# Optimization experiments

Measured on AMD Instinct MI355X. Metric: run time of the kernel, lower is better.

The kernel has to match this reference:

```python
import jax, jax.numpy as jnp
import numpy as np

N_CELL, N_NET, N_GCELL = 50000, 10000, 20000
E = 100000
D = 32   # hidden_node = hidden_net = hidden_hanna = out_node = out_net
DP = 16  # hidden_pin = hidden_edge feats


def setup_inputs() -> dict:
    key = jax.random.key(0)
    ks = jax.random.split(key, 21)
    f = jax.random.normal
    ri = lambda k, n: jax.random.randint(k, (E,), 0, n, dtype=jnp.int32)
    return {
        'node_feat': f(ks[0], (N_CELL, D), jnp.float32),
        'net_feat': f(ks[1], (N_NET, D), jnp.float32),
        'pin_feat': f(ks[2], (E, DP), jnp.float32),
        'hanna_feat': f(ks[3], (N_GCELL, D), jnp.float32),
        'edge_feat': f(ks[4], (E, DP), jnp.float32),
        'pins_src': ri(ks[5], N_CELL), 'pins_dst': ri(ks[6], N_NET),
        'pinned_src': ri(ks[7], N_NET), 'pinned_dst': ri(ks[8], N_CELL),
        'connect_src': ri(ks[9], N_GCELL), 'connect_dst': ri(ks[10], N_GCELL),
        'pt_src': ri(ks[11], N_CELL), 'pt_dst': ri(ks[12], N_GCELL),
        'pf_src': ri(ks[13], N_GCELL), 'pf_dst': ri(ks[14], N_CELL),
        'W_net': f(ks[15], (D, D)) * 0.1, 'b_net': jnp.zeros((D,), jnp.float32),
        'W_topo': f(ks[16], (DP, D * D)) * 0.1, 'b_topo': jnp.zeros((D * D,), jnp.float32),
        'W_pins': f(ks[17], (D, D)) * 0.1, 'b_pins': jnp.zeros((D,), jnp.float32),
        'W_connect': f(ks[18], (D, D)) * 0.1, 'b_connect': jnp.zeros((D,), jnp.float32),
        'W_pt': f(ks[19], (D, D)) * 0.1, 'b_pt': jnp.zeros((D,), jnp.float32),
        'b_pinned': jnp.zeros((D,), jnp.float32), 'b_pf': jnp.zeros((D,), jnp.float32),
    }


def _deg(idx, n):
    # clamped degree, as DGL clamps to min 1
    return jnp.maximum(jax.ops.segment_sum(jnp.ones_like(idx, jnp.float32), idx, n), 1.0)


def graph_conv(h_src, W, b, src, dst, n_src, n_dst):
    # DGL GraphConv with norm='both': D_out^{-1/2} gather -> sum -> D_in^{-1/2}, then W, b
    feat = (h_src * _deg(src, n_src)[:, None] ** -0.5) @ W
    agg = jax.ops.segment_sum(feat[src], dst, n_dst)
    return agg * _deg(dst, n_dst)[:, None] ** -0.5 + b


def nn_conv(h_src, efeat, W_topo, b_topo, bias, src, dst, n_dst):
    # DGL NNConv (aggregator='mean'): per-edge weight from edge_func, mean over in-edges
    d_in = h_src.shape[1]
    w = (efeat @ W_topo + b_topo).reshape(-1, d_in, bias.shape[0])  # (E, d_in, d_out)
    m = jnp.einsum('ei,eio->eo', h_src[src], w)
    return jax.ops.segment_sum(m, dst, n_dst) / _deg(dst, n_dst)[:, None] + bias


def reference(node_feat, net_feat, pin_feat, hanna_feat, edge_feat,
              pins_src, pins_dst, pinned_src, pinned_dst, connect_src, connect_dst,
              pt_src, pt_dst, pf_src, pf_dst,
              W_net, b_net, W_topo, b_topo, W_pins, b_pins,
              W_connect, b_connect, W_pt, b_pt, b_pinned, b_pf):
    # 'pins': cell -> net (GraphConv)
    h_net = graph_conv(node_feat, W_pins, b_pins, pins_src, pins_dst, N_CELL, N_NET)
    # 'pinned': net -> cell (NNConv) + 'point-from': gcell -> cell (NNConv); agg='sum'
    h_cell = (nn_conv(net_feat, pin_feat, W_topo, b_topo, b_pinned, pinned_src, pinned_dst, N_CELL)
              + nn_conv(hanna_feat, edge_feat, W_topo, b_topo, b_pf, pf_src, pf_dst, N_CELL))
    # 'connect': gcell -> gcell + 'point-to': cell -> gcell (GraphConvs); agg='sum'
    h_gcell = (graph_conv(hanna_feat, W_connect, b_connect, connect_src, connect_dst, N_GCELL, N_GCELL)
               + graph_conv(node_feat, W_pt, b_pt, pt_src, pt_dst, N_CELL, N_GCELL))
    return (h_cell, h_net + net_feat @ W_net + b_net, h_gcell)
```

## Files before the change

### kernel.cpp

```cpp
#include <hip/hip_runtime.h>

typedef unsigned short u16;
typedef unsigned int u32;

#define NC 50000
#define NN 10000
#define NG 20000
#define NE 100000
#define NSCAN 150016
#define NBLK 74


__device__ __forceinline__ float bflo(u32 a) { return __uint_as_float(a << 16); }
__device__ __forceinline__ float bfhi(u32 a) { return __uint_as_float(a & 0xFFFF0000u); }
__device__ __forceinline__ u16 fbf(float f) {
  u32 u = __float_as_uint(f);
  return (u16)((u + 0x7FFFu + ((u >> 16) & 1u)) >> 16);
}

__device__ __forceinline__ float nn_msg(int e, int s, const float* __restrict__ ef,
                                        const u16* __restrict__ T,
                                        const float* __restrict__ C, int o) {
  const float4* efp = reinterpret_cast<const float4*>(ef + (size_t)e * 16);
  float4 ea = efp[0], eb = efp[1], ec = efp[2], ed = efp[3];
  const uint4* tp = reinterpret_cast<const uint4*>(T + (size_t)s * 512 + o * 16);
  uint4 ta = tp[0], tb = tp[1];
  float m = C[(size_t)s * 32 + o];
  m += ea.x * bflo(ta.x) + ea.y * bfhi(ta.x) + ea.z * bflo(ta.y) + ea.w * bfhi(ta.y);
  m += eb.x * bflo(ta.z) + eb.y * bfhi(ta.z) + eb.z * bflo(ta.w) + eb.w * bfhi(ta.w);
  m += ec.x * bflo(tb.x) + ec.y * bfhi(tb.x) + ec.z * bflo(tb.y) + ec.w * bfhi(tb.y);
  m += ed.x * bflo(tb.z) + ed.y * bfhi(tb.z) + ed.z * bflo(tb.w) + ed.w * bfhi(tb.w);
  return m;
}

__global__ __launch_bounds__(512) void k_front(
    const float* __restrict__ feat_net, const float* __restrict__ feat_han,
    const float* __restrict__ W_topo, const float* __restrict__ b_topo,
    u16* __restrict__ T_net, u16* __restrict__ T_han,
    float* __restrict__ C_net, float* __restrict__ C_han,
    const int* __restrict__ pins_src, const int* __restrict__ pins_dst,
    const int* __restrict__ pinned_dst, const int* __restrict__ pf_dst,
    const int* __restrict__ connect_src, const int* __restrict__ connect_dst,
    const int* __restrict__ pt_src, const int* __restrict__ pt_dst,
    int* __restrict__ hist, int* __restrict__ srccnt) {
  int b = blockIdx.x;
  int tid = threadIdx.x;
  if (b < 938) {
    __shared__ float hs[4][32];
    bool han = b >= 313;
    const float* feat = han ? feat_han : feat_net;
    u16* T = han ? T_han : T_net;
    int n = han ? NG : NN;
    int blk = han ? (b - 313) : b;
    int j = tid;
    int p = j & 15, o = j >> 4;
    float w[32];
#pragma unroll
    for (int i = 0; i < 32; i++) w[i] = W_topo[p * 1024 + i * 32 + o];
    int s0 = blk * 32;
    int s1 = min(s0 + 32, n);
    for (int s = s0; s < s1; s += 4) {
      __syncthreads();
      if (tid < 128) {
        int r = tid >> 5, i = tid & 31;
        int sn = s + r;
        hs[r][i] = (sn < s1) ? feat[(size_t)sn * 32 + i] : 0.f;
      }
      __syncthreads();
#pragma unroll
      for (int r = 0; r < 4; r++) {
        int sn = s + r;
        if (sn >= s1) break;
        float acc = 0.f;
#pragma unroll
        for (int i = 0; i < 32; i++) acc += hs[r][i] * w[i];
        T[(size_t)sn * 512 + j] = fbf(acc);
      }
    }
    return;
  }
  if (b < 2813) {
    int t = (b - 938) * 512 + tid;
    int s2 = t >> 5, o = t & 31;
    bool han = s2 >= NN;
    const float* feat = han ? feat_han : feat_net;
    float* C = han ? C_han : C_net;
    int s = han ? s2 - NN : s2;
    float acc = 0.f;
#pragma unroll 8
    for (int i = 0; i < 32; i++)
      acc += feat[(size_t)s * 32 + i] * b_topo[i * 32 + o];
    C[(size_t)s * 32 + o] = acc;
    return;
  }
  int e = (b - 2813) * 512 + tid;
  if (e >= NE) return;
  atomicAdd(&hist[pins_dst[e]], 1);
  atomicAdd(&hist[10000 + connect_dst[e]], 1);
  atomicAdd(&hist[30000 + pt_dst[e]], 1);
  atomicAdd(&hist[50000 + pinned_dst[e]], 1);
  atomicAdd(&hist[100000 + pf_dst[e]], 1);
  atomicAdd(&srccnt[pins_src[e]], 1);
  atomicAdd(&srccnt[50000 + connect_src[e]], 1);
  atomicAdd(&srccnt[70000 + pt_src[e]], 1);
}

__global__ __launch_bounds__(256) void k_scan(
    const int* __restrict__ cnt, int* __restrict__ bases,
    int* __restrict__ cursor) {
  __shared__ int sm[256];
  __shared__ int carryS;
  int b = blockIdx.x, tid = threadIdx.x;
  int lim = b * 2048;
  int part = 0;
  for (int i = tid * 4; i < lim; i += 1024) {
    int4 v = *reinterpret_cast<const int4*>(cnt + i);
    part += v.x + v.y + v.z + v.w;
  }
  sm[tid] = part;
  __syncthreads();
  for (int off = 128; off > 0; off >>= 1) {
    if (tid < off) sm[tid] += sm[tid + off];
    __syncthreads();
  }
  if (tid == 0) carryS = sm[0];
  __syncthreads();
  int base = b * 2048 + tid * 8;
  int v[8];
  int tot = 0;
#pragma unroll
  for (int j = 0; j < 8; j++) {
    int i = base + j;
    v[j] = (i < NSCAN) ? cnt[i] : 0;
    tot += v[j];
  }
  sm[tid] = tot;
  __syncthreads();
  for (int off = 1; off < 256; off <<= 1) {
    int add = (tid >= off) ? sm[tid - off] : 0;
    __syncthreads();
    sm[tid] += add;
    __syncthreads();
  }
  int excl = sm[tid] - tot + carryS;
#pragma unroll
  for (int j = 0; j < 8; j++) {
    int i = base + j;
    if (i < NSCAN) { bases[i] = excl; cursor[i] = excl; }
    excl += v[j];
  }
}

__global__ __launch_bounds__(512) void k_fill(
    const int* __restrict__ pins_src, const int* __restrict__ pins_dst,
    const int* __restrict__ connect_src, const int* __restrict__ connect_dst,
    const int* __restrict__ pt_src, const int* __restrict__ pt_dst,
    const int* __restrict__ pinned_src, const int* __restrict__ pinned_dst,
    const int* __restrict__ pf_src, const int* __restrict__ pf_dst,
    const int* __restrict__ srccnt, int* __restrict__ cursor,
    int2* __restrict__ csr_gc, int2* __restrict__ csr_nn) {
  int t = blockIdx.x * 512 + threadIdx.x;
  if (t >= 5 * NE) return;
  int r = (t >= NE) + (t >= 2 * NE) + (t >= 3 * NE) + (t >= 4 * NE);
  int e = t - r * NE;
  const int* srcs = r == 0 ? pins_src : r == 1 ? connect_src
                   : r == 2 ? pt_src : r == 3 ? pinned_src : pf_src;
  const int* dsts = r == 0 ? pins_dst : r == 1 ? connect_dst
                   : r == 2 ? pt_dst : r == 3 ? pinned_dst : pf_dst;
  int off = r == 0 ? 0 : r == 1 ? 10000 : r == 2 ? 30000 : r == 3 ? 50000 : 100000;
  int s = srcs[e];
  int g = off + dsts[e];
  int pos = atomicAdd(&cursor[g], 1);
  if (r < 3) {
    int soff = r == 0 ? 0 : r == 1 ? 50000 : 70000;
    float w = rsqrtf(fmaxf((float)srccnt[soff + s], 1.f));
    csr_gc[pos] = make_int2(s, __float_as_int(w));
  } else {
    csr_nn[pos - 300000] = make_int2(e, s);
  }
}

__global__ __launch_bounds__(512) void k_big(
    const int* __restrict__ hist, const int* __restrict__ bases,
    const int2* __restrict__ csr_gc, const int2* __restrict__ csr_nn,
    const float* __restrict__ node_feat, const float* __restrict__ hanna_feat,
    const float* __restrict__ net_feat,
    const float* __restrict__ pin_feat, const float* __restrict__ edge_feat,
    const u16* __restrict__ T_net, const u16* __restrict__ T_han,
    const float* __restrict__ C_net, const float* __restrict__ C_han,
    const float* __restrict__ b_pinned, const float* __restrict__ b_pf,
    const float* __restrict__ W_pins, const float* __restrict__ b_pins,
    const float* __restrict__ W_net, const float* __restrict__ b_net,
    const float* __restrict__ W_connect, const float* __restrict__ b_connect,
    const float* __restrict__ W_pt, const float* __restrict__ b_pt,
    float* __restrict__ out) {
  __shared__ float Wa[1024], Wb[1024];
  __shared__ float srow[16][32];
  int b = blockIdx.x, tid = threadIdx.x;
  if (b < 3125) {
    int t = b * 512 + tid;
    int d = t >> 5, o = t & 31;
    float a0 = 0.f, a1 = 0.f;
    {
      int g = 50000 + d;
      int base = bases[g] - 300000, deg = hist[g];
      int k = 0;
      for (; k + 1 < deg; k += 2) {
        int2 ea = csr_nn[base + k], eb = csr_nn[base + k + 1];
        a0 += nn_msg(ea.x, ea.y, pin_feat, T_net, C_net, o) +
              nn_msg(eb.x, eb.y, pin_feat, T_net, C_net, o);
      }
      if (k < deg) {
        int2 ea = csr_nn[base + k];
        a0 += nn_msg(ea.x, ea.y, pin_feat, T_net, C_net, o);
      }
      a0 /= fmaxf((float)deg, 1.f);
    }
    {
      int g = 100000 + d;
      int base = bases[g] - 300000, deg = hist[g];
      int k = 0;
      for (; k + 1 < deg; k += 2) {
        int2 ea = csr_nn[base + k], eb = csr_nn[base + k + 1];
        a1 += nn_msg(ea.x, ea.y, edge_feat, T_han, C_han, o) +
              nn_msg(eb.x, eb.y, edge_feat, T_han, C_han, o);
      }
      if (k < deg) {
        int2 ea = csr_nn[base + k];
        a1 += nn_msg(ea.x, ea.y, edge_feat, T_han, C_han, o);
      }
      a1 /= fmaxf((float)deg, 1.f);
    }
    out[(size_t)d * 32 + o] = a0 + a1 + b_pinned[o] + b_pf[o];
    return;
  }
  if (b < 3750) {
    int bb = b - 3125;
    for (int k = tid; k < 1024; k += 512) {
      Wa[k] = W_pins[k];
      Wb[k] = W_net[k];
    }
    int rl = tid >> 5, o = tid & 31;
    int r = bb * 16 + rl;
    int base = bases[r], deg = hist[r];
    float acc = 0.f;
    int k = 0;
    for (; k + 1 < deg; k += 2) {
      int2 pa = csr_gc[base + k], pb = csr_gc[base + k + 1];
      acc += node_feat[(size_t)pa.x * 32 + o] * __int_as_float(pa.y) +
             node_feat[(size_t)pb.x * 32 + o] * __int_as_float(pb.y);
    }
    if (k < deg) {
      int2 pa = csr_gc[base + k];
      acc += node_feat[(size_t)pa.x * 32 + o] * __int_as_float(pa.y);
    }
    srow[rl][o] = acc;
    __syncthreads();
    float a1 = 0.f, a2 = 0.f;
#pragma unroll 8
    for (int i = 0; i < 32; i++) {
      a1 += srow[rl][i] * Wa[i * 32 + o];
      a2 += net_feat[(size_t)r * 32 + i] * Wb[i * 32 + o];
    }
    out[1600000 + (size_t)r * 32 + o] =
        a1 * rsqrtf(fmaxf((float)deg, 1.f)) + b_pins[o] + a2 + b_net[o];
    return;
  }
  int bb = b - 3750;
  for (int k = tid; k < 1024; k += 512) {
    Wa[k] = W_connect[k];
    Wb[k] = W_pt[k];
  }
  int rl = tid >> 6;
  int half = (tid >> 5) & 1;
  int o = tid & 31;
  int r = bb * 8 + rl;
  int g = (half ? 30000 : 10000) + r;
  const float* feat = half ? node_feat : hanna_feat;
  int base = bases[g], deg = hist[g];
  float acc = 0.f;
  int k = 0;
  for (; k + 1 < deg; k += 2) {
    int2 pa = csr_gc[base + k], pb = csr_gc[base + k + 1];
    acc += feat[(size_t)pa.x * 32 + o] * __int_as_float(pa.y) +
           feat[(size_t)pb.x * 32 + o] * __int_as_float(pb.y);
  }
  if (k < deg) {
    int2 pa = csr_gc[base + k];
    acc += feat[(size_t)pa.x * 32 + o] * __int_as_float(pa.y);
  }
  srow[rl * 2 + half][o] = acc;
  __syncthreads();
  if (half == 0) {
    float a1 = 0.f, a2 = 0.f;
#pragma unroll 8
    for (int i = 0; i < 32; i++) {
      a1 += srow[rl * 2 + 0][i] * Wa[i * 32 + o];
      a2 += srow[rl * 2 + 1][i] * Wb[i * 32 + o];
    }
    out[1920000 + (size_t)r * 32 + o] =
        a1 * rsqrtf(fmaxf((float)hist[10000 + r], 1.f)) + b_connect[o] +
        a2 * rsqrtf(fmaxf((float)hist[30000 + r], 1.f)) + b_pt[o];
  }
}

extern "C" void kernel_launch(void* const* d_in, const int* in_sizes, int n_in,
                              void* d_out, int out_size, void* d_ws, size_t ws_size,
                              hipStream_t stream) {
  const float* node_feat  = (const float*)d_in[0];
  const float* net_feat   = (const float*)d_in[1];
  const float* pin_feat   = (const float*)d_in[2];
  const float* hanna_feat = (const float*)d_in[3];
  const float* edge_feat  = (const float*)d_in[4];
  const int* pins_src    = (const int*)d_in[5];
  const int* pins_dst    = (const int*)d_in[6];
  const int* pinned_src  = (const int*)d_in[7];
  const int* pinned_dst  = (const int*)d_in[8];
  const int* connect_src = (const int*)d_in[9];
  const int* connect_dst = (const int*)d_in[10];
  const int* pt_src      = (const int*)d_in[11];
  const int* pt_dst      = (const int*)d_in[12];
  const int* pf_src      = (const int*)d_in[13];
  const int* pf_dst      = (const int*)d_in[14];
  const float* W_net     = (const float*)d_in[15];
  const float* b_net     = (const float*)d_in[16];
  const float* W_topo    = (const float*)d_in[17];
  const float* b_topo    = (const float*)d_in[18];
  const float* W_pins    = (const float*)d_in[19];
  const float* b_pins    = (const float*)d_in[20];
  const float* W_connect = (const float*)d_in[21];
  const float* b_connect = (const float*)d_in[22];
  const float* W_pt      = (const float*)d_in[23];
  const float* b_pt      = (const float*)d_in[24];
  const float* b_pinned  = (const float*)d_in[25];
  const float* b_pf      = (const float*)d_in[26];
  float* out = (float*)d_out;

  int* wi = (int*)d_ws;
  int* hist    = wi + 0;
  int* srccnt  = wi + 150016;
  int* bases   = wi + 270032;
  int* cursor  = wi + 420048;
  int2* csr_gc = (int2*)(wi + 570064);
  int2* csr_nn = (int2*)(wi + 1170064);
  float* wf = (float*)d_ws;
  float* C_net  = wf + 1570064;
  float* C_han  = wf + 1890064;
  u16* T_net = (u16*)((char*)d_ws + 10120256);
  u16* T_han = (u16*)((char*)d_ws + 10120256 + 10240000);

  hipMemsetAsync(d_ws, 0, 270032 * sizeof(int), stream);

  k_front<<<3009, 512, 0, stream>>>(
      net_feat, hanna_feat, W_topo, b_topo, T_net, T_han, C_net, C_han,
      pins_src, pins_dst, pinned_dst, pf_dst, connect_src, connect_dst,
      pt_src, pt_dst, hist, srccnt);

  k_scan<<<NBLK, 256, 0, stream>>>(hist, bases, cursor);

  k_fill<<<(5 * NE + 511) / 512, 512, 0, stream>>>(
      pins_src, pins_dst, connect_src, connect_dst, pt_src, pt_dst,
      pinned_src, pinned_dst, pf_src, pf_dst, srccnt, cursor,
      csr_gc, csr_nn);

  k_big<<<6250, 512, 0, stream>>>(
      hist, bases, csr_gc, csr_nn, node_feat, hanna_feat, net_feat,
      pin_feat, edge_feat, T_net, T_han, C_net, C_han, b_pinned, b_pf,
      W_pins, b_pins, W_net, b_net, W_connect, b_connect, W_pt, b_pt, out);
}
```

Baseline: 323.2 us.

## Fuse four kernels into one persistent kernel with grid-wide barriers

Replaces the four kernel launches (front, scan, fill, big) with one persistent kernel of 512 blocks that loops over the former block indices and separates the phases with an atomic-counter grid barrier. The aim is to remove per-launch overhead and the idle tails between dependent kernels. The scan now uses 512 threads with 4 elements each, and the two NNConv aggregation loops are interleaved in one loop. The barrier assumes all 512 blocks are resident at once, which launch_bounds(512,4) is meant to allow. Fixing the grid at 512 blocks of 512 threads may lower occupancy in the gather-heavy final phase.

```diff
diff --git a/kernel.cpp b/kernel.cpp
--- a/kernel.cpp
+++ b/kernel.cpp
@@ -9,6 +9,7 @@
 #define NE 100000
 #define NSCAN 150016
 #define NBLK 74
+#define NGRID 512
 
 
 __device__ __forceinline__ float bflo(u32 a) { return __uint_as_float(a << 16); }
@@ -33,274 +34,261 @@
   return m;
 }
 
-__global__ __launch_bounds__(512) void k_front(
-    const float* __restrict__ feat_net, const float* __restrict__ feat_han,
-    const float* __restrict__ W_topo, const float* __restrict__ b_topo,
-    u16* __restrict__ T_net, u16* __restrict__ T_han,
-    float* __restrict__ C_net, float* __restrict__ C_han,
+__device__ __forceinline__ void gbar(int* cnt) {
+  __syncthreads();
+  if (threadIdx.x == 0) {
+    __threadfence();
+    atomicAdd(cnt, 1);
+    while (atomicAdd(cnt, 0) < NGRID) __builtin_amdgcn_s_sleep(8);
+  }
+  __syncthreads();
+  __threadfence();
+}
+
+__global__ __launch_bounds__(512, 4) void k_mega(
+    const float* __restrict__ node_feat, const float* __restrict__ net_feat,
+    const float* __restrict__ pin_feat, const float* __restrict__ hanna_feat,
+    const float* __restrict__ edge_feat,
     const int* __restrict__ pins_src, const int* __restrict__ pins_dst,
-    const int* __restrict__ pinned_dst, const int* __restrict__ pf_dst,
+    const int* __restrict__ pinned_src, const int* __restrict__ pinned_dst,
     const int* __restrict__ connect_src, const int* __restrict__ connect_dst,
     const int* __restrict__ pt_src, const int* __restrict__ pt_dst,
-    int* __restrict__ hist, int* __restrict__ srccnt) {
-  int b = blockIdx.x;
-  int tid = threadIdx.x;
-  if (b < 938) {
-    __shared__ float hs[4][32];
-    bool han = b >= 313;
-    const float* feat = han ? feat_han : feat_net;
-    u16* T = han ? T_han : T_net;
-    int n = han ? NG : NN;
-    int blk = han ? (b - 313) : b;
-    int j = tid;
-    int p = j & 15, o = j >> 4;
-    float w[32];
-#pragma unroll
-    for (int i = 0; i < 32; i++) w[i] = W_topo[p * 1024 + i * 32 + o];
-    int s0 = blk * 32;
-    int s1 = min(s0 + 32, n);
-    for (int s = s0; s < s1; s += 4) {
-      __syncthreads();
-      if (tid < 128) {
-        int r = tid >> 5, i = tid & 31;
-        int sn = s + r;
-        hs[r][i] = (sn < s1) ? feat[(size_t)sn * 32 + i] : 0.f;
-      }
-      __syncthreads();
-#pragma unroll
-      for (int r = 0; r < 4; r++) {
-        int sn = s + r;
-        if (sn >= s1) break;
-        float acc = 0.f;
-#pragma unroll
-        for (int i = 0; i < 32; i++) acc += hs[r][i] * w[i];
-        T[(size_t)sn * 512 + j] = fbf(acc);
-      }
-    }
-    return;
-  }
-  if (b < 2813) {
-    int t = (b - 938) * 512 + tid;
-    int s2 = t >> 5, o = t & 31;
-    bool han = s2 >= NN;
-    const float* feat = han ? feat_han : feat_net;
-    float* C = han ? C_han : C_net;
-    int s = han ? s2 - NN : s2;
-    float acc = 0.f;
-#pragma unroll 8
-    for (int i = 0; i < 32; i++)
-      acc += feat[(size_t)s * 32 + i] * b_topo[i * 32 + o];
-    C[(size_t)s * 32 + o] = acc;
-    return;
-  }
-  int e = (b - 2813) * 512 + tid;
-  if (e >= NE) return;
-  atomicAdd(&hist[pins_dst[e]], 1);
-  atomicAdd(&hist[10000 + connect_dst[e]], 1);
-  atomicAdd(&hist[30000 + pt_dst[e]], 1);
-  atomicAdd(&hist[50000 + pinned_dst[e]], 1);
-  atomicAdd(&hist[100000 + pf_dst[e]], 1);
-  atomicAdd(&srccnt[pins_src[e]], 1);
-  atomicAdd(&srccnt[50000 + connect_src[e]], 1);
-  atomicAdd(&srccnt[70000 + pt_src[e]], 1);
-}
-
-__global__ __launch_bounds__(256) void k_scan(
-    const int* __restrict__ cnt, int* __restrict__ bases,
-    int* __restrict__ cursor) {
-  __shared__ int sm[256];
-  __shared__ int carryS;
-  int b = blockIdx.x, tid = threadIdx.x;
-  int lim = b * 2048;
-  int part = 0;
-  for (int i = tid * 4; i < lim; i += 1024) {
-    int4 v = *reinterpret_cast<const int4*>(cnt + i);
-    part += v.x + v.y + v.z + v.w;
-  }
-  sm[tid] = part;
-  __syncthreads();
-  for (int off = 128; off > 0; off >>= 1) {
-    if (tid < off) sm[tid] += sm[tid + off];
-    __syncthreads();
-  }
-  if (tid == 0) carryS = sm[0];
-  __syncthreads();
-  int base = b * 2048 + tid * 8;
-  int v[8];
-  int tot = 0;
-#pragma unroll
-  for (int j = 0; j < 8; j++) {
-    int i = base + j;
-    v[j] = (i < NSCAN) ? cnt[i] : 0;
-    tot += v[j];
-  }
-  sm[tid] = tot;
-  __syncthreads();
-  for (int off = 1; off < 256; off <<= 1) {
-    int add = (tid >= off) ? sm[tid - off] : 0;
-    __syncthreads();
-    sm[tid] += add;
-    __syncthreads();
-  }
-  int excl = sm[tid] - tot + carryS;
-#pragma unroll
-  for (int j = 0; j < 8; j++) {
-    int i = base + j;
-    if (i < NSCAN) { bases[i] = excl; cursor[i] = excl; }
-    excl += v[j];
-  }
-}
-
-__global__ __launch_bounds__(512) void k_fill(
-    const int* __restrict__ pins_src, const int* __restrict__ pins_dst,
-    const int* __restrict__ connect_src, const int* __restrict__ connect_dst,
-    const int* __restrict__ pt_src, const int* __restrict__ pt_dst,
-    const int* __restrict__ pinned_src, const int* __restrict__ pinned_dst,
     const int* __restrict__ pf_src, const int* __restrict__ pf_dst,
-    const int* __restrict__ srccnt, int* __restrict__ cursor,
-    int2* __restrict__ csr_gc, int2* __restrict__ csr_nn) {
-  int t = blockIdx.x * 512 + threadIdx.x;
-  if (t >= 5 * NE) return;
-  int r = (t >= NE) + (t >= 2 * NE) + (t >= 3 * NE) + (t >= 4 * NE);
-  int e = t - r * NE;
-  const int* srcs = r == 0 ? pins_src : r == 1 ? connect_src
-                   : r == 2 ? pt_src : r == 3 ? pinned_src : pf_src;
-  const int* dsts = r == 0 ? pins_dst : r == 1 ? connect_dst
-                   : r == 2 ? pt_dst : r == 3 ? pinned_dst : pf_dst;
-  int off = r == 0 ? 0 : r == 1 ? 10000 : r == 2 ? 30000 : r == 3 ? 50000 : 100000;
-  int s = srcs[e];
-  int g = off + dsts[e];
-  int pos = atomicAdd(&cursor[g], 1);
-  if (r < 3) {
-    int soff = r == 0 ? 0 : r == 1 ? 50000 : 70000;
-    float w = rsqrtf(fmaxf((float)srccnt[soff + s], 1.f));
-    csr_gc[pos] = make_int2(s, __float_as_int(w));
-  } else {
-    csr_nn[pos - 300000] = make_int2(e, s);
-  }
-}
-
-__global__ __launch_bounds__(512) void k_big(
-    const int* __restrict__ hist, const int* __restrict__ bases,
-    const int2* __restrict__ csr_gc, const int2* __restrict__ csr_nn,
-    const float* __restrict__ node_feat, const float* __restrict__ hanna_feat,
-    const float* __restrict__ net_feat,
-    const float* __restrict__ pin_feat, const float* __restrict__ edge_feat,
-    const u16* __restrict__ T_net, const u16* __restrict__ T_han,
-    const float* __restrict__ C_net, const float* __restrict__ C_han,
-    const float* __restrict__ b_pinned, const float* __restrict__ b_pf,
+    const float* __restrict__ W_net, const float* __restrict__ b_net,
+    const float* __restrict__ W_topo, const float* __restrict__ b_topo,
     const float* __restrict__ W_pins, const float* __restrict__ b_pins,
-    const float* __restrict__ W_net, const float* __restrict__ b_net,
     const float* __restrict__ W_connect, const float* __restrict__ b_connect,
     const float* __restrict__ W_pt, const float* __restrict__ b_pt,
+    const float* __restrict__ b_pinned, const float* __restrict__ b_pf,
+    int* __restrict__ hist, int* __restrict__ srccnt, int* __restrict__ bar,
+    int* __restrict__ bases, int* __restrict__ cursor,
+    int2* __restrict__ csr_gc, int2* __restrict__ csr_nn,
+    float* __restrict__ C_net, float* __restrict__ C_han,
+    u16* __restrict__ T_net, u16* __restrict__ T_han,
     float* __restrict__ out) {
+  __shared__ float hs[4][32];
+  __shared__ int smi[512];
   __shared__ float Wa[1024], Wb[1024];
   __shared__ float srow[16][32];
-  int b = blockIdx.x, tid = threadIdx.x;
-  if (b < 3125) {
-    int t = b * 512 + tid;
-    int d = t >> 5, o = t & 31;
-    float a0 = 0.f, a1 = 0.f;
-    {
-      int g = 50000 + d;
-      int base = bases[g] - 300000, deg = hist[g];
+  int tid = threadIdx.x;
+
+  for (int vb = blockIdx.x; vb < 3009; vb += NGRID) {
+    if (vb < 938) {
+      bool han = vb >= 313;
+      const float* feat = han ? hanna_feat : net_feat;
+      u16* T = han ? T_han : T_net;
+      int n = han ? NG : NN;
+      int blk = han ? (vb - 313) : vb;
+      int j = tid;
+      int p = j & 15, o = j >> 4;
+      float w[32];
+#pragma unroll
+      for (int i = 0; i < 32; i++) w[i] = W_topo[p * 1024 + i * 32 + o];
+      int s0 = blk * 32;
+      int s1 = min(s0 + 32, n);
+      for (int s = s0; s < s1; s += 4) {
+        __syncthreads();
+        if (tid < 128) {
+          int r = tid >> 5, i = tid & 31;
+          int sn = s + r;
+          hs[r][i] = (sn < s1) ? feat[(size_t)sn * 32 + i] : 0.f;
+        }
+        __syncthreads();
+#pragma unroll
+        for (int r = 0; r < 4; r++) {
+          int sn = s + r;
+          if (sn >= s1) break;
+          float acc = 0.f;
+#pragma unroll
+          for (int i = 0; i < 32; i++) acc += hs[r][i] * w[i];
+          T[(size_t)sn * 512 + j] = fbf(acc);
+        }
+      }
+    } else if (vb < 2813) {
+      int t = (vb - 938) * 512 + tid;
+      int s2 = t >> 5, o = t & 31;
+      bool han = s2 >= NN;
+      const float* feat = han ? hanna_feat : net_feat;
+      float* C = han ? C_han : C_net;
+      int s = han ? s2 - NN : s2;
+      float acc = 0.f;
+#pragma unroll 8
+      for (int i = 0; i < 32; i++)
+        acc += feat[(size_t)s * 32 + i] * b_topo[i * 32 + o];
+      C[(size_t)s * 32 + o] = acc;
+    } else {
+      int e = (vb - 2813) * 512 + tid;
+      if (e < NE) {
+        atomicAdd(&hist[pins_dst[e]], 1);
+        atomicAdd(&hist[10000 + connect_dst[e]], 1);
+        atomicAdd(&hist[30000 + pt_dst[e]], 1);
+        atomicAdd(&hist[50000 + pinned_dst[e]], 1);
+        atomicAdd(&hist[100000 + pf_dst[e]], 1);
+        atomicAdd(&srccnt[pins_src[e]], 1);
+        atomicAdd(&srccnt[50000 + connect_src[e]], 1);
+        atomicAdd(&srccnt[70000 + pt_src[e]], 1);
+      }
+    }
+  }
+  gbar(&bar[0]);
+
+  for (int vb = blockIdx.x; vb < NBLK; vb += NGRID) {
+    int lim = vb * 2048;
+    int part = 0;
+    for (int i = tid * 4; i < lim; i += 2048) {
+      int4 v = *reinterpret_cast<const int4*>(hist + i);
+      part += v.x + v.y + v.z + v.w;
+    }
+    smi[tid] = part;
+    __syncthreads();
+    for (int off = 256; off > 0; off >>= 1) {
+      if (tid < off) smi[tid] += smi[tid + off];
+      __syncthreads();
+    }
+    int carry = smi[0];
+    __syncthreads();
+    int base = vb * 2048 + tid * 4;
+    int v[4];
+    int tot = 0;
+#pragma unroll
+    for (int j = 0; j < 4; j++) {
+      int i = base + j;
+      v[j] = (i < NSCAN) ? hist[i] : 0;
+      tot += v[j];
+    }
+    smi[tid] = tot;
+    __syncthreads();
+    for (int off = 1; off < 512; off <<= 1) {
+      int add = (tid >= off) ? smi[tid - off] : 0;
+      __syncthreads();
+      smi[tid] += add;
+      __syncthreads();
+    }
+    int excl = smi[tid] - tot + carry;
+#pragma unroll
+    for (int j = 0; j < 4; j++) {
+      int i = base + j;
+      if (i < NSCAN) { bases[i] = excl; cursor[i] = excl; }
+      excl += v[j];
+    }
+  }
+  gbar(&bar[1]);
+
+  for (int vb = blockIdx.x; vb < 977; vb += NGRID) {
+    int t = vb * 512 + tid;
+    if (t < 5 * NE) {
+      int r = (t >= NE) + (t >= 2 * NE) + (t >= 3 * NE) + (t >= 4 * NE);
+      int e = t - r * NE;
+      const int* srcs = r == 0 ? pins_src : r == 1 ? connect_src
+                       : r == 2 ? pt_src : r == 3 ? pinned_src : pf_src;
+      const int* dsts = r == 0 ? pins_dst : r == 1 ? connect_dst
+                       : r == 2 ? pt_dst : r == 3 ? pinned_dst : pf_dst;
+      int off = r == 0 ? 0 : r == 1 ? 10000 : r == 2 ? 30000
+              : r == 3 ? 50000 : 100000;
+      int s = srcs[e];
+      int g = off + dsts[e];
+      int pos = atomicAdd(&cursor[g], 1);
+      if (r < 3) {
+        int soff = r == 0 ? 0 : r == 1 ? 50000 : 70000;
+        float w = rsqrtf(fmaxf((float)srccnt[soff + s], 1.f));
+        csr_gc[pos] = make_int2(s, __float_as_int(w));
+      } else {
+        csr_nn[pos - 300000] = make_int2(e, s);
+      }
+    }
+  }
+  gbar(&bar[2]);
+
+  for (int vb = blockIdx.x; vb < 6250; vb += NGRID) {
+    if (vb < 3125) {
+      int t = vb * 512 + tid;
+      int d = t >> 5, o = t & 31;
+      int g0 = 50000 + d, g1 = 100000 + d;
+      int b0 = bases[g0] - 300000, d0 = hist[g0];
+      int b1 = bases[g1] - 300000, d1 = hist[g1];
+      float a0 = 0.f, a1 = 0.f;
+      int kmax = max(d0, d1);
+      for (int k = 0; k < kmax; k++) {
+        int2 ea = make_int2(0, 0), eb = make_int2(0, 0);
+        bool h0 = k < d0, h1 = k < d1;
+        if (h0) ea = csr_nn[b0 + k];
+        if (h1) eb = csr_nn[b1 + k];
+        if (h0) a0 += nn_msg(ea.x, ea.y, pin_feat, T_net, C_net, o);
+        if (h1) a1 += nn_msg(eb.x, eb.y, edge_feat, T_han, C_han, o);
+      }
+      a0 /= fmaxf((float)d0, 1.f);
+      a1 /= fmaxf((float)d1, 1.f);
+      out[(size_t)d * 32 + o] = a0 + a1 + b_pinned[o] + b_pf[o];
+    } else if (vb < 3750) {
+      __syncthreads();
+      int bb = vb - 3125;
+      for (int k = tid; k < 1024; k += 512) {
+        Wa[k] = W_pins[k];
+        Wb[k] = W_net[k];
+      }
+      int rl = tid >> 5, o = tid & 31;
+      int r = bb * 16 + rl;
+      int base = bases[r], deg = hist[r];
+      float acc = 0.f;
       int k = 0;
       for (; k + 1 < deg; k += 2) {
-        int2 ea = csr_nn[base + k], eb = csr_nn[base + k + 1];
-        a0 += nn_msg(ea.x, ea.y, pin_feat, T_net, C_net, o) +
-              nn_msg(eb.x, eb.y, pin_feat, T_net, C_net, o);
+        int2 pa = csr_gc[base + k], pb = csr_gc[base + k + 1];
+        acc += node_feat[(size_t)pa.x * 32 + o] * __int_as_float(pa.y) +
+               node_feat[(size_t)pb.x * 32 + o] * __int_as_float(pb.y);
       }
       if (k < deg) {
-        int2 ea = csr_nn[base + k];
-        a0 += nn_msg(ea.x, ea.y, pin_feat, T_net, C_net, o);
-      }
-      a0 /= fmaxf((float)deg, 1.f);
-    }
-    {
-      int g = 100000 + d;
-      int base = bases[g] - 300000, deg = hist[g];
+        int2 pa = csr_gc[base + k];
+        acc += node_feat[(size_t)pa.x * 32 + o] * __int_as_float(pa.y);
+      }
+      srow[rl][o] = acc;
+      __syncthreads();
+      float a1 = 0.f, a2 = 0.f;
+#pragma unroll 8
+      for (int i = 0; i < 32; i++) {
+        a1 += srow[rl][i] * Wa[i * 32 + o];
+        a2 += net_feat[(size_t)r * 32 + i] * Wb[i * 32 + o];
+      }
+      out[1600000 + (size_t)r * 32 + o] =
+          a1 * rsqrtf(fmaxf((float)deg, 1.f)) + b_pins[o] + a2 + b_net[o];
+    } else {
+      __syncthreads();
+      int bb = vb - 3750;
+      for (int k = tid; k < 1024; k += 512) {
+        Wa[k] = W_connect[k];
+        Wb[k] = W_pt[k];
+      }
+      int rl = tid >> 6;
+      int half = (tid >> 5) & 1;
+      int o = tid & 31;
+      int r = bb * 8 + rl;
+      int g = (half ? 30000 : 10000) + r;
+      const float* feat = half ? node_feat : hanna_feat;
+      int base = bases[g], deg = hist[g];
+      float acc = 0.f;
       int k = 0;
       for (; k + 1 < deg; k += 2) {
-        int2 ea = csr_nn[base + k], eb = csr_nn[base + k + 1];
-        a1 += nn_msg(ea.x, ea.y, edge_feat, T_han, C_han, o) +
-              nn_msg(eb.x, eb.y, edge_feat, T_han, C_han, o);
+        int2 pa = csr_gc[base + k], pb = csr_gc[base + k + 1];
+        acc += feat[(size_t)pa.x * 32 + o] * __int_as_float(pa.y) +
+               feat[(size_t)pb.x * 32 + o] * __int_as_float(pb.y);
       }
       if (k < deg) {
-        int2 ea = csr_nn[base + k];
-        a1 += nn_msg(ea.x, ea.y, edge_feat, T_han, C_han, o);
-      }
-      a1 /= fmaxf((float)deg, 1.f);
-    }
-    out[(size_t)d * 32 + o] = a0 + a1 + b_pinned[o] + b_pf[o];
-    return;
-  }
-  if (b < 3750) {
-    int bb = b - 3125;
-    for (int k = tid; k < 1024; k += 512) {
-      Wa[k] = W_pins[k];
-      Wb[k] = W_net[k];
-    }
-    int rl = tid >> 5, o = tid & 31;
-    int r = bb * 16 + rl;
-    int base = bases[r], deg = hist[r];
-    float acc = 0.f;
-    int k = 0;
-    for (; k + 1 < deg; k += 2) {
-      int2 pa = csr_gc[base + k], pb = csr_gc[base + k + 1];
-      acc += node_feat[(size_t)pa.x * 32 + o] * __int_as_float(pa.y) +
-             node_feat[(size_t)pb.x * 32 + o] * __int_as_float(pb.y);
-    }
-    if (k < deg) {
-      int2 pa = csr_gc[base + k];
-      acc += node_feat[(size_t)pa.x * 32 + o] * __int_as_float(pa.y);
-    }
-    srow[rl][o] = acc;
-    __syncthreads();
-    float a1 = 0.f, a2 = 0.f;
+        int2 pa = csr_gc[base + k];
+        acc += feat[(size_t)pa.x * 32 + o] * __int_as_float(pa.y);
+      }
+      srow[rl * 2 + half][o] = acc;
+      __syncthreads();
+      if (half == 0) {
+        float a1 = 0.f, a2 = 0.f;
 #pragma unroll 8
-    for (int i = 0; i < 32; i++) {
-      a1 += srow[rl][i] * Wa[i * 32 + o];
-      a2 += net_feat[(size_t)r * 32 + i] * Wb[i * 32 + o];
-    }
-    out[1600000 + (size_t)r * 32 + o] =
-        a1 * rsqrtf(fmaxf((float)deg, 1.f)) + b_pins[o] + a2 + b_net[o];
-    return;
-  }
-  int bb = b - 3750;
-  for (int k = tid; k < 1024; k += 512) {
-    Wa[k] = W_connect[k];
-    Wb[k] = W_pt[k];
-  }
-  int rl = tid >> 6;
-  int half = (tid >> 5) & 1;
-  int o = tid & 31;
-  int r = bb * 8 + rl;
-  int g = (half ? 30000 : 10000) + r;
-  const float* feat = half ? node_feat : hanna_feat;
-  int base = bases[g], deg = hist[g];
-  float acc = 0.f;
-  int k = 0;
-  for (; k + 1 < deg; k += 2) {
-    int2 pa = csr_gc[base + k], pb = csr_gc[base + k + 1];
-    acc += feat[(size_t)pa.x * 32 + o] * __int_as_float(pa.y) +
-           feat[(size_t)pb.x * 32 + o] * __int_as_float(pb.y);
-  }
-  if (k < deg) {
-    int2 pa = csr_gc[base + k];
-    acc += feat[(size_t)pa.x * 32 + o] * __int_as_float(pa.y);
-  }
-  srow[rl * 2 + half][o] = acc;
-  __syncthreads();
-  if (half == 0) {
-    float a1 = 0.f, a2 = 0.f;
-#pragma unroll 8
-    for (int i = 0; i < 32; i++) {
-      a1 += srow[rl * 2 + 0][i] * Wa[i * 32 + o];
-      a2 += srow[rl * 2 + 1][i] * Wb[i * 32 + o];
-    }
-    out[1920000 + (size_t)r * 32 + o] =
-        a1 * rsqrtf(fmaxf((float)hist[10000 + r], 1.f)) + b_connect[o] +
-        a2 * rsqrtf(fmaxf((float)hist[30000 + r], 1.f)) + b_pt[o];
+        for (int i = 0; i < 32; i++) {
+          a1 += srow[rl * 2 + 0][i] * Wa[i * 32 + o];
+          a2 += srow[rl * 2 + 1][i] * Wb[i * 32 + o];
+        }
+        out[1920000 + (size_t)r * 32 + o] =
+            a1 * rsqrtf(fmaxf((float)hist[10000 + r], 1.f)) + b_connect[o] +
+            a2 * rsqrtf(fmaxf((float)hist[30000 + r], 1.f)) + b_pt[o];
+      }
+    }
   }
 }
 
@@ -339,32 +327,25 @@
   int* wi = (int*)d_ws;
   int* hist    = wi + 0;
   int* srccnt  = wi + 150016;
-  int* bases   = wi + 270032;
-  int* cursor  = wi + 420048;
-  int2* csr_gc = (int2*)(wi + 570064);
-  int2* csr_nn = (int2*)(wi + 1170064);
+  int* bar     = wi + 270032;
+  int* bases   = wi + 270040;
+  int* cursor  = wi + 420056;
+  int2* csr_gc = (int2*)(wi + 570072);
+  int2* csr_nn = (int2*)(wi + 1170072);
   float* wf = (float*)d_ws;
-  float* C_net  = wf + 1570064;
-  float* C_han  = wf + 1890064;
-  u16* T_net = (u16*)((char*)d_ws + 10120256);
-  u16* T_han = (u16*)((char*)d_ws + 10120256 + 10240000);
-
-  hipMemsetAsync(d_ws, 0, 270032 * sizeof(int), stream);
-
-  k_front<<<3009, 512, 0, stream>>>(
-      net_feat, hanna_feat, W_topo, b_topo, T_net, T_han, C_net, C_han,
-      pins_src, pins_dst, pinned_dst, pf_dst, connect_src, connect_dst,
-      pt_src, pt_dst, hist, srccnt);
-
-  k_scan<<<NBLK, 256, 0, stream>>>(hist, bases, cursor);
-
-  k_fill<<<(5 * NE + 511) / 512, 512, 0, stream>>>(
-      pins_src, pins_dst, connect_src, connect_dst, pt_src, pt_dst,
-      pinned_src, pinned_dst, pf_src, pf_dst, srccnt, cursor,
-      csr_gc, csr_nn);
-
-  k_big<<<6250, 512, 0, stream>>>(
-      hist, bases, csr_gc, csr_nn, node_feat, hanna_feat, net_feat,
-      pin_feat, edge_feat, T_net, T_han, C_net, C_han, b_pinned, b_pf,
-      W_pins, b_pins, W_net, b_net, W_connect, b_connect, W_pt, b_pt, out);
-}
+  float* C_net  = wf + 1570072;
+  float* C_han  = wf + 1890072;
+  u16* T_net = (u16*)((char*)d_ws + 10120320);
+  u16* T_han = (u16*)((char*)d_ws + 10120320 + 10240000);
+
+  hipMemsetAsync(d_ws, 0, 270040 * sizeof(int), stream);
+
+  k_mega<<<NGRID, 512, 0, stream>>>(
+      node_feat, net_feat, pin_feat, hanna_feat, edge_feat,
+      pins_src, pins_dst, pinned_src, pinned_dst, connect_src, connect_dst,
+      pt_src, pt_dst, pf_src, pf_dst,
+      W_net, b_net, W_topo, b_topo, W_pins, b_pins,
+      W_connect, b_connect, W_pt, b_pt, b_pinned, b_pf,
+      hist, srccnt, bar, bases, cursor, csr_gc, csr_nn,
+      C_net, C_han, T_net, T_han, out);
+}
```

Measured after the change: 612.0 us. 89.3% more time.
